# Kernel optimization log

Measured on AMD Instinct MI355X. Metric: run time of the kernel, lower is better.

The kernel has to match this reference:

```python
import jax, jax.numpy as jnp
import numpy as np

NMS_THR = 0.5
SCORE_THR = 0.05
MAX_BOXES = 300
N_ANCHORS = 5000
N_CLASSES = 80
IMG = 640.0  # image size used to scale synthetic box coords


def setup_inputs() -> dict:
    key = jax.random.key(0)
    k1, k2, k3 = jax.random.split(key, 3)
    # build well-formed boxes (x1<=x2, y1<=y2) in a 640x640 image
    c1 = jax.random.uniform(k1, (1, N_ANCHORS, 2), jnp.float32) * IMG
    c2 = jax.random.uniform(k2, (1, N_ANCHORS, 2), jnp.float32) * IMG
    boxes = jnp.concatenate([jnp.minimum(c1, c2), jnp.maximum(c1, c2) + 1.0], axis=-1)
    # classification scores in [0,1], squared to skew toward low values like sigmoid logits
    classification = jax.random.uniform(k3, (1, N_ANCHORS, N_CLASSES), jnp.float32) ** 2
    return {"boxes": boxes, "classification": classification}


def _iou_matrix(b):
    # b: [N,4] as (x1,y1,x2,y2) -> [N,N] pairwise IoU
    x1, y1, x2, y2 = b[:, 0], b[:, 1], b[:, 2], b[:, 3]
    area = (x2 - x1) * (y2 - y1)
    iw = jnp.maximum(jnp.minimum(x2[:, None], x2[None, :]) - jnp.maximum(x1[:, None], x1[None, :]), 0.0)
    ih = jnp.maximum(jnp.minimum(y2[:, None], y2[None, :]) - jnp.maximum(y1[:, None], y1[None, :]), 0.0)
    inter = iw * ih
    union = area[:, None] + area[None, :] - inter
    return inter / jnp.maximum(union, 1e-8)


def _nms_one_class(scores, iou):
    # greedy NMS for one class; scores: [N], iou: [N,N] (shared across classes)
    n = scores.shape[0]
    order = jnp.argsort(-scores)          # descending score order
    valid = scores > SCORE_THR            # per-class score-threshold filter
    idxs = jnp.arange(n)

    def step(carry, oi):
        suppressed, kept, count = carry
        alive = (~suppressed[oi]) & valid[oi] & (count < MAX_BOXES)
        # a kept box suppresses all others with IoU above threshold
        suppressed = suppressed | (alive & (iou[oi] > NMS_THR) & (idxs != oi))
        kept = kept.at[oi].set(alive)
        return (suppressed, kept, count + alive.astype(jnp.int32)), None

    init = (jnp.zeros(n, jnp.bool_), jnp.zeros(n, jnp.bool_), jnp.int32(0))
    (_, kept, _), _ = jax.lax.scan(step, init, order)
    return kept  # [N] bool mask in original index space


def reference(boxes, classification):
    b = boxes[0]             # [N,4]
    cls = classification[0]  # [N,C]
    iou = _iou_matrix(b)     # [N,N], class-independent
    kept = jax.vmap(_nms_one_class, in_axes=(1, None))(cls, iou)  # [C,N]
    # scatter surviving scores back to dense per-class score map (zeros elsewhere)
    selected = jnp.where(kept.T, cls, 0.0)                        # [N,C]
    detections = jnp.concatenate([b, selected], axis=1)           # [N,4+C]
    return detections[None]                                       # [1,N,4+C]
```

## Files before the change

### kernel.cpp

```cpp
#include <hip/hip_runtime.h>

#define N_ANCHORS 5000
#define N_CLASSES 80
#define OUT_COLS  84
#define MAX_BOXES 300
#define SCORE_THR 0.05f

#define LK_PAD    5120
#define NB        4096
#define BLOCK     1024
#define SLOTS     8
#define DONEP     0x40000000u
#define NIW       6
#define NSW       9

typedef unsigned long long u64;
typedef unsigned int u32;

#define WG __HIP_MEMORY_SCOPE_WORKGROUP

__device__ __forceinline__ float readlane_f(float v, int l) {
    return __int_as_float(__builtin_amdgcn_readlane(__float_as_int(v), l));
}
__device__ __forceinline__ u32 aload(u32* p) {
    return __hip_atomic_load(p, __ATOMIC_ACQUIRE, WG);
}
__device__ __forceinline__ u64 aload64(u64* p) {
    return __hip_atomic_load(p, __ATOMIC_ACQUIRE, WG);
}
__device__ __forceinline__ int bucket_of(float s) {
    float u = sqrtf(s);
    int b = (int)((u - 0.2236f) * 5275.0f);
    return (NB - 1) - min(max(b, 0), NB - 1);
}
__device__ __forceinline__ bool iou3(float4 a, float aa, float4 q, float aq) {
    float iw = fmaxf(fminf(a.z, q.z) - fmaxf(a.x, q.x), 0.0f);
    float ih = fmaxf(fminf(a.w, q.w) - fmaxf(a.y, q.y), 0.0f);
    return 3.0f * (iw * ih) > aa + aq;
}

__global__ __launch_bounds__(BLOCK, 1) void nms(const float* __restrict__ cls,
                                                const float4* __restrict__ boxes4,
                                                float* __restrict__ out) {
    __shared__ __align__(16) char SMEM[63680];
    u64*    lk      = (u64*)SMEM;
    u32*    hist    = (u32*)(SMEM + 40960);
    u64*    Iring   = (u64*)(SMEM + 40960);
    float4* Bring   = (float4*)(SMEM + 45056);
    u64*    kout    = (u64*)(SMEM + 53248);
    float4* kbox    = (float4*)(SMEM + 57344);
    float*  karea   = (float*)(SMEM + 62208);
    u64*    KS      = (u64*)(SMEM + 63424);
    u32*    wtot    = (u32*)(SMEM + 63488);
    u64*    flagIK  = (u64*)(SMEM + 63552);
    u32*    flagIK32= (u32*)(SMEM + 63552);
    u64*    progcnt = (u64*)(SMEM + 63616);

    const int c = blockIdx.x;
    const int t = threadIdx.x;
    const int lane = t & 63;
    const int wv = t >> 6;
    const float* boxesf = (const float*)boxes4;

    u32 sb[5];
    #pragma unroll
    for (int m = 0; m < 5; ++m) {
        int j = m * BLOCK + t;
        float v = (j < N_ANCHORS) ? cls[(size_t)j * N_CLASSES + c] : 0.0f;
        sb[m] = (v > SCORE_THR) ? __float_as_uint(v) : 0u;
    }
    for (int i = t; i < N_ANCHORS; i += BLOCK)
        out[(size_t)i * OUT_COLS + 4 + c] = 0.0f;
    if (c < 4)
        for (int i = t; i < N_ANCHORS; i += BLOCK)
            out[(size_t)i * OUT_COLS + c] = boxesf[(size_t)i * 4 + c];

    for (int b = t; b < NB; b += BLOCK) hist[b] = 0u;
    if (t < 304) { kbox[t] = make_float4(1e9f, 1e9f, 1e9f, 1e9f); karea[t] = 1e18f; }
    if (t < SLOTS) flagIK[t] = 0ull;
    if (t == 0) *progcnt = 0ull;
    __syncthreads();
    #pragma unroll
    for (int m = 0; m < 5; ++m)
        if (sb[m]) atomicAdd(&hist[bucket_of(__uint_as_float(sb[m]))], 1u);
    __syncthreads();

    const int hbase = t * 4;
    u32 vals[4]; u32 run = 0;
    #pragma unroll
    for (int k = 0; k < 4; ++k) { run += hist[hbase + k]; vals[k] = run; }
    u32 x = run;
    #pragma unroll
    for (int off = 1; off < 64; off <<= 1) { u32 y = __shfl_up(x, off); if (lane >= off) x += y; }
    if (lane == 63) wtot[wv] = x;
    __syncthreads();
    u32 woff = 0;
    for (int w = 0; w < wv; ++w) woff += wtot[w];
    const u32 exb = woff + x - run;
    #pragma unroll
    for (int k = 0; k < 4; ++k) hist[hbase + k] = exb + (k ? vals[k - 1] : 0u);
    __syncthreads();
    #pragma unroll
    for (int m = 0; m < 5; ++m) {
        if (sb[m]) {
            int j = m * BLOCK + t;
            u32 pos = atomicAdd(&hist[bucket_of(__uint_as_float(sb[m]))], 1u);
            lk[pos] = ((u64)sb[m] << 32) | (u32)(~(u32)j);
        }
    }
    __syncthreads();
    const int total = (int)hist[NB - 1];
    for (int v = total + t; v < LK_PAD; v += BLOCK) lk[v] = 0ull;
    for (int b = hbase; b < hbase + 4; ++b) {
        int s0 = b ? (int)hist[b - 1] : 0;
        int e  = (int)hist[b];
        for (int i = s0 + 1; i < e; ++i) {
            u64 key = lk[i]; int q = i - 1;
            while (q >= s0 && lk[q] < key) { lk[q + 1] = lk[q]; --q; }
            lk[q + 1] = key;
        }
    }
    __syncthreads();
    const int nch = (total + 63) >> 6;

    if (wv >= 1 && wv <= NIW) {
        for (int j = wv - 1; j < nch; j += NIW) {
            const int slot = j & (SLOTS - 1);
            u64 e = lk[j * 64 + lane];
            u32 jj = e ? ~(u32)e : 0u;
            float4 bx = boxes4[jj];
            float ar = (bx.z - bx.x) * (bx.w - bx.y);
            u32 p;
            for (;;) {
                p = (u32)aload64(progcnt);
                if ((int)p >= j - (SLOTS - 1)) break;
                __builtin_amdgcn_s_sleep(2);
            }
            if (p >= DONEP) return;
            u64 word = 0ull;
            #pragma unroll 16
            for (int q = 0; q < 64; ++q) {
                float4 o;
                o.x = readlane_f(bx.x, q); o.y = readlane_f(bx.y, q);
                o.z = readlane_f(bx.z, q); o.w = readlane_f(bx.w, q);
                float aq = readlane_f(ar, q);
                float iw = fmaxf(fminf(bx.z, o.z) - fmaxf(bx.x, o.x), 0.0f);
                float ih = fmaxf(fminf(bx.w, o.w) - fmaxf(bx.y, o.y), 0.0f);
                if (3.0f * (iw * ih) > ar + aq) word |= (1ull << q);
            }
            Iring[slot * 64 + lane] = word;
            if (lane == 0)
                __hip_atomic_store(&flagIK32[slot * 2 + 1], (u32)(j + 1), __ATOMIC_RELEASE, WG);
        }
        return;
    }
    if (wv > NIW) {
        for (int j = wv - (NIW + 1); j < nch; j += NSW) {
            const int slot = j & (SLOTS - 1);
            u64 e = lk[j * 64 + lane];
            bool validL = (e != 0ull);
            u32 jj = validL ? ~(u32)e : 0u;
            float4 bx = boxes4[jj];
            float ar = (bx.z - bx.x) * (bx.w - bx.y);
            u64 pk;
            for (;;) {
                pk = aload64(progcnt);
                if ((int)(u32)pk >= j - (SLOTS - 1)) break;
                __builtin_amdgcn_s_sleep(2);
            }
            if ((u32)pk >= DONEP) return;
            Bring[slot * 64 + lane] = bx;
            bool sup = !validL;
            u32 ka = (u32)(pk >> 32);
            for (u32 r = 0; r < ka; r += 4) {
                float4 q0 = kbox[r], q1 = kbox[r + 1], q2 = kbox[r + 2], q3 = kbox[r + 3];
                float4 a4 = *(const float4*)(karea + r);
                sup = sup | iou3(bx, ar, q0, a4.x) | iou3(bx, ar, q1, a4.y)
                          | iou3(bx, ar, q2, a4.z) | iou3(bx, ar, q3, a4.w);
                if ((r & 28u) == 28u && !__ballot(!sup)) break;
            }
            for (;;) {
                pk = aload64(progcnt);
                if ((int)(u32)pk >= j - 2) break;
                __builtin_amdgcn_s_sleep(1);
            }
            u32 p = (u32)pk;
            u32 kb2 = (u32)(pk >> 32);
            if (kb2 < ka) kb2 = ka;
            u32 r1 = (kb2 + 3) & ~3u;
            for (u32 r = ka & ~3u; r < r1; r += 4) {
                float4 q0 = kbox[r], q1 = kbox[r + 1], q2 = kbox[r + 2], q3 = kbox[r + 3];
                float4 a4 = *(const float4*)(karea + r);
                sup = sup | iou3(bx, ar, q0, a4.x) | iou3(bx, ar, q1, a4.y)
                          | iou3(bx, ar, q2, a4.z) | iou3(bx, ar, q3, a4.w);
            }
            u64 ksf = __ballot(sup);
            if (lane == 0) {
                KS[slot] = ksf;
                __hip_atomic_store(&flagIK32[slot * 2], (u32)(j + 1), __ATOMIC_RELEASE, WG);
            }
            if (p >= DONEP) return;
        }
        return;
    }

    int kept = 0; u32 kcur = 0; bool capped = false;
    u64 kmPrev = 0ull;
    float4 bxPrev = make_float4(0.f, 0.f, 0.f, 0.f);
    float arPrev = 0.f;
    u64 key = lk[lane];
    for (int k = 0; k < nch; ++k) {
        const int slot = k & (SLOTS - 1);
        bool valid = (key != 0ull);
        u32 j = valid ? ~(u32)key : 0u;
        float sc = __uint_as_float((u32)(key >> 32));

        const u64 want = ((u64)(u32)(k + 1) << 32) | (u32)(k + 1);
        while (aload64(&flagIK[slot]) != want) { }
        u64 km = 0ull;
        u64 ks = KS[slot];
        if (ks != ~0ull) {
            float4 bx = Bring[slot * 64 + lane];
            u64 I = Iring[slot * 64 + lane];
            float ar = (bx.z - bx.x) * (bx.w - bx.y);
            bool alive = valid && !((ks >> lane) & 1ull);
            u64 mk = kmPrev;
            while (mk) {
                int pos = __ffsll((long long)mk) - 1; mk &= mk - 1;
                float qx = readlane_f(bxPrev.x, pos), qy = readlane_f(bxPrev.y, pos);
                float qz = readlane_f(bxPrev.z, pos), qw = readlane_f(bxPrev.w, pos);
                float aq = readlane_f(arPrev, pos);
                float iw = fmaxf(fminf(bx.z, qz) - fmaxf(bx.x, qx), 0.0f);
                float ih = fmaxf(fminf(bx.w, qw) - fmaxf(bx.y, qy), 0.0f);
                alive = alive && !(3.0f * (iw * ih) > ar + aq);
            }
            u64 rem = __ballot(alive);
            if (rem) {
                while (rem) {
                    int pos = __ffsll((long long)rem) - 1;
                    km |= 1ull << pos;
                    if (++kept == MAX_BOXES) { capped = true; break; }
                    u32 lo = (u32)__builtin_amdgcn_readlane((int)(u32)I, pos);
                    u32 hi = (u32)__builtin_amdgcn_readlane((int)(u32)(I >> 32), pos);
                    rem &= ~(((u64)hi << 32) | (u64)lo);
                }
                if ((km >> lane) & 1ull) {
                    int rank = (int)__popcll(km & ((1ull << lane) - 1ull));
                    kbox[kcur + rank] = bx;
                    karea[kcur + rank] = ar;
                    kout[kcur + rank] = ((u64)__float_as_uint(sc) << 32) | j;
                }
                kcur += (u32)__popcll(km);
            }
            bxPrev = bx; arPrev = ar;
        }
        kmPrev = km;
        if (capped) break;
        if (lane == 0)
            __hip_atomic_store(progcnt, ((u64)kcur << 32) | (u32)(k + 1),
                               __ATOMIC_RELEASE, WG);
        key = lk[(k + 1) * 64 + lane];
    }
    if (lane == 0)
        __hip_atomic_store(progcnt, ((u64)kcur << 32) | DONEP, __ATOMIC_RELEASE, WG);

    for (u32 i = (u32)lane; i < kcur; i += 64) {
        u64 e = kout[i];
        out[(size_t)((u32)e) * OUT_COLS + 4 + c] = __uint_as_float((u32)(e >> 32));
    }
}

extern "C" void kernel_launch(void* const* d_in, const int* in_sizes, int n_in,
                              void* d_out, int out_size, void* d_ws, size_t ws_size,
                              hipStream_t stream) {
    const float* cls = (const float*)d_in[1];
    float* out = (float*)d_out;
    nms<<<N_CLASSES, BLOCK, 0, stream>>>(cls, (const float4*)d_in[0], out);
}
```

Baseline: 147.1 us.

## Process two 64-box chunks per pipeline step in NMS wavefront pipeline

```diff
diff --git a/kernel.cpp b/kernel.cpp
--- a/kernel.cpp
+++ b/kernel.cpp
@@ -9,21 +9,30 @@
 #define LK_PAD    5120
 #define NB        4096
 #define BLOCK     1024
-#define SLOTS     8
+#define SLOTS     4
 #define DONEP     0x40000000u
 #define NIW       6
 #define NSW       9
 
 typedef unsigned long long u64;
 typedef unsigned int u32;
+typedef unsigned short u16;
 
 #define WG __HIP_MEMORY_SCOPE_WORKGROUP
 
 __device__ __forceinline__ float readlane_f(float v, int l) {
     return __int_as_float(__builtin_amdgcn_readlane(__float_as_int(v), l));
 }
-__device__ __forceinline__ u32 aload(u32* p) {
-    return __hip_atomic_load(p, __ATOMIC_ACQUIRE, WG);
+__device__ __forceinline__ u64 readlane_u64(u64 v, int l) {
+    u32 lo = (u32)__builtin_amdgcn_readlane((int)(u32)v, l);
+    u32 hi = (u32)__builtin_amdgcn_readlane((int)(u32)(v >> 32), l);
+    return ((u64)hi << 32) | lo;
+}
+__device__ __forceinline__ float4 bcast4(float4 b, int q) {
+    float4 o;
+    o.x = readlane_f(b.x, q); o.y = readlane_f(b.y, q);
+    o.z = readlane_f(b.z, q); o.w = readlane_f(b.w, q);
+    return o;
 }
 __device__ __forceinline__ u64 aload64(u64* p) {
     return __hip_atomic_load(p, __ATOMIC_ACQUIRE, WG);
@@ -42,19 +51,19 @@
 __global__ __launch_bounds__(BLOCK, 1) void nms(const float* __restrict__ cls,
                                                 const float4* __restrict__ boxes4,
                                                 float* __restrict__ out) {
-    __shared__ __align__(16) char SMEM[63680];
+    __shared__ __align__(16) char SMEM[63552];
     u64*    lk      = (u64*)SMEM;
     u32*    hist    = (u32*)(SMEM + 40960);
     u64*    Iring   = (u64*)(SMEM + 40960);
     float4* Bring   = (float4*)(SMEM + 45056);
-    u64*    kout    = (u64*)(SMEM + 53248);
+    u16*    kout16  = (u16*)(SMEM + 53248);
+    u64*    KS      = (u64*)(SMEM + 53856);
     float4* kbox    = (float4*)(SMEM + 57344);
     float*  karea   = (float*)(SMEM + 62208);
-    u64*    KS      = (u64*)(SMEM + 63424);
-    u32*    wtot    = (u32*)(SMEM + 63488);
-    u64*    flagIK  = (u64*)(SMEM + 63552);
-    u32*    flagIK32= (u32*)(SMEM + 63552);
-    u64*    progcnt = (u64*)(SMEM + 63616);
+    u32*    wtot    = (u32*)(SMEM + 63424);
+    u64*    flagIK  = (u64*)(SMEM + 63488);
+    u32*    flagIK32= (u32*)(SMEM + 63488);
+    u64*    progcnt = (u64*)(SMEM + 63520);
 
     const int c = blockIdx.x;
     const int t = threadIdx.x;
@@ -121,152 +130,179 @@
         }
     }
     __syncthreads();
-    const int nch = (total + 63) >> 6;
+    const int nsteps = (total + 127) >> 7;
 
     if (wv >= 1 && wv <= NIW) {
-        for (int j = wv - 1; j < nch; j += NIW) {
-            const int slot = j & (SLOTS - 1);
-            u64 e = lk[j * 64 + lane];
-            u32 jj = e ? ~(u32)e : 0u;
-            float4 bx = boxes4[jj];
-            float ar = (bx.z - bx.x) * (bx.w - bx.y);
+        for (int s = wv - 1; s < nsteps; s += NIW) {
+            const int slot = s & (SLOTS - 1);
+            u64 eA = lk[s * 128 + lane], eB = lk[s * 128 + 64 + lane];
+            u32 jA = eA ? ~(u32)eA : 0u, jB = eB ? ~(u32)eB : 0u;
+            float4 bA = boxes4[jA], bB = boxes4[jB];
+            float aA = (bA.z - bA.x) * (bA.w - bA.y);
+            float aB = (bB.z - bB.x) * (bB.w - bB.y);
+            u64 AA = 0ull, BB = 0ull;
+            #pragma unroll 16
+            for (int q = 0; q < 64; ++q) {
+                float4 oA = bcast4(bA, q); float qaA = readlane_f(aA, q);
+                float4 oB = bcast4(bB, q); float qaB = readlane_f(aB, q);
+                if (iou3(bA, aA, oA, qaA)) AA |= 1ull << q;
+                if (iou3(bB, aB, oB, qaB)) BB |= 1ull << q;
+            }
             u32 p;
             for (;;) {
                 p = (u32)aload64(progcnt);
-                if ((int)p >= j - (SLOTS - 1)) break;
+                if ((int)p >= s - (SLOTS - 1)) break;
                 __builtin_amdgcn_s_sleep(2);
             }
             if (p >= DONEP) return;
-            u64 word = 0ull;
-            #pragma unroll 16
-            for (int q = 0; q < 64; ++q) {
-                float4 o;
-                o.x = readlane_f(bx.x, q); o.y = readlane_f(bx.y, q);
-                o.z = readlane_f(bx.z, q); o.w = readlane_f(bx.w, q);
-                float aq = readlane_f(ar, q);
-                float iw = fmaxf(fminf(bx.z, o.z) - fmaxf(bx.x, o.x), 0.0f);
-                float ih = fmaxf(fminf(bx.w, o.w) - fmaxf(bx.y, o.y), 0.0f);
-                if (3.0f * (iw * ih) > ar + aq) word |= (1ull << q);
-            }
-            Iring[slot * 64 + lane] = word;
+            Iring[(slot * 64 + lane) * 2]     = AA;
+            Iring[(slot * 64 + lane) * 2 + 1] = BB;
             if (lane == 0)
-                __hip_atomic_store(&flagIK32[slot * 2 + 1], (u32)(j + 1), __ATOMIC_RELEASE, WG);
+                __hip_atomic_store(&flagIK32[slot * 2 + 1], (u32)(s + 1), __ATOMIC_RELEASE, WG);
         }
         return;
     }
     if (wv > NIW) {
-        for (int j = wv - (NIW + 1); j < nch; j += NSW) {
-            const int slot = j & (SLOTS - 1);
-            u64 e = lk[j * 64 + lane];
-            bool validL = (e != 0ull);
-            u32 jj = validL ? ~(u32)e : 0u;
-            float4 bx = boxes4[jj];
-            float ar = (bx.z - bx.x) * (bx.w - bx.y);
-            u64 pk;
+        for (int s = wv - (NIW + 1); s < nsteps; s += NSW) {
+            const int slot = s & (SLOTS - 1);
+            u64 eA = lk[s * 128 + lane], eB = lk[s * 128 + 64 + lane];
+            bool vA = (eA != 0ull), vB = (eB != 0ull);
+            u32 jA = vA ? ~(u32)eA : 0u, jB = vB ? ~(u32)eB : 0u;
+            float4 bA = boxes4[jA], bB = boxes4[jB];
+            float aA = (bA.z - bA.x) * (bA.w - bA.y);
+            float aB = (bB.z - bB.x) * (bB.w - bB.y);
+            bool supA = !vA, supB = !vB;
+            bool allsup = false;
+            u64 pk = aload64(progcnt);
+            u32 kn = (u32)(pk >> 32), done = 0;
+            {
+                u32 r1 = (kn + 3) & ~3u;
+                for (u32 r = done; r < r1; r += 4) {
+                    float4 q0 = kbox[r], q1 = kbox[r+1], q2 = kbox[r+2], q3 = kbox[r+3];
+                    float4 a4 = *(const float4*)(karea + r);
+                    supA = supA | iou3(bA,aA,q0,a4.x) | iou3(bA,aA,q1,a4.y)
+                                | iou3(bA,aA,q2,a4.z) | iou3(bA,aA,q3,a4.w);
+                    supB = supB | iou3(bB,aB,q0,a4.x) | iou3(bB,aB,q1,a4.y)
+                                | iou3(bB,aB,q2,a4.z) | iou3(bB,aB,q3,a4.w);
+                    if (((r >> 2) & 7u) == 7u && !__ballot(!(supA && supB))) { allsup = true; break; }
+                }
+                done = kn & ~3u;
+            }
             for (;;) {
                 pk = aload64(progcnt);
-                if ((int)(u32)pk >= j - (SLOTS - 1)) break;
+                if ((int)(u32)pk >= s - (SLOTS - 1)) break;
                 __builtin_amdgcn_s_sleep(2);
             }
             if ((u32)pk >= DONEP) return;
-            Bring[slot * 64 + lane] = bx;
-            bool sup = !validL;
-            u32 ka = (u32)(pk >> 32);
-            for (u32 r = 0; r < ka; r += 4) {
-                float4 q0 = kbox[r], q1 = kbox[r + 1], q2 = kbox[r + 2], q3 = kbox[r + 3];
-                float4 a4 = *(const float4*)(karea + r);
-                sup = sup | iou3(bx, ar, q0, a4.x) | iou3(bx, ar, q1, a4.y)
-                          | iou3(bx, ar, q2, a4.z) | iou3(bx, ar, q3, a4.w);
-                if ((r & 28u) == 28u && !__ballot(!sup)) break;
-            }
-            for (;;) {
+            Bring[slot * 128 + lane] = bA;
+            Bring[slot * 128 + 64 + lane] = bB;
+            while (!allsup) {
+                kn = (u32)(pk >> 32);
+                u32 r1 = (kn + 3) & ~3u;
+                for (u32 r = done; r < r1; r += 4) {
+                    float4 q0 = kbox[r], q1 = kbox[r+1], q2 = kbox[r+2], q3 = kbox[r+3];
+                    float4 a4 = *(const float4*)(karea + r);
+                    supA = supA | iou3(bA,aA,q0,a4.x) | iou3(bA,aA,q1,a4.y)
+                                | iou3(bA,aA,q2,a4.z) | iou3(bA,aA,q3,a4.w);
+                    supB = supB | iou3(bB,aB,q0,a4.x) | iou3(bB,aB,q1,a4.y)
+                                | iou3(bB,aB,q2,a4.z) | iou3(bB,aB,q3,a4.w);
+                    if (((r >> 2) & 7u) == 7u && !__ballot(!(supA && supB))) { allsup = true; break; }
+                }
+                if (allsup) break;
+                done = kn & ~3u;
+                if ((int)(u32)pk >= s - 1) break;
                 pk = aload64(progcnt);
-                if ((int)(u32)pk >= j - 2) break;
-                __builtin_amdgcn_s_sleep(1);
-            }
-            u32 p = (u32)pk;
-            u32 kb2 = (u32)(pk >> 32);
-            if (kb2 < ka) kb2 = ka;
-            u32 r1 = (kb2 + 3) & ~3u;
-            for (u32 r = ka & ~3u; r < r1; r += 4) {
-                float4 q0 = kbox[r], q1 = kbox[r + 1], q2 = kbox[r + 2], q3 = kbox[r + 3];
-                float4 a4 = *(const float4*)(karea + r);
-                sup = sup | iou3(bx, ar, q0, a4.x) | iou3(bx, ar, q1, a4.y)
-                          | iou3(bx, ar, q2, a4.z) | iou3(bx, ar, q3, a4.w);
-            }
-            u64 ksf = __ballot(sup);
+            }
+            u64 KSA = __ballot(supA), KSB = __ballot(supB);
             if (lane == 0) {
-                KS[slot] = ksf;
-                __hip_atomic_store(&flagIK32[slot * 2], (u32)(j + 1), __ATOMIC_RELEASE, WG);
-            }
-            if (p >= DONEP) return;
+                KS[slot * 2] = KSA; KS[slot * 2 + 1] = KSB;
+                __hip_atomic_store(&flagIK32[slot * 2], (u32)(s + 1), __ATOMIC_RELEASE, WG);
+            }
+            if ((u32)pk >= DONEP) return;
         }
         return;
     }
 
     int kept = 0; u32 kcur = 0; bool capped = false;
-    u64 kmPrev = 0ull;
-    float4 bxPrev = make_float4(0.f, 0.f, 0.f, 0.f);
-    float arPrev = 0.f;
-    u64 key = lk[lane];
-    for (int k = 0; k < nch; ++k) {
-        const int slot = k & (SLOTS - 1);
-        bool valid = (key != 0ull);
-        u32 j = valid ? ~(u32)key : 0u;
-        float sc = __uint_as_float((u32)(key >> 32));
-
-        const u64 want = ((u64)(u32)(k + 1) << 32) | (u32)(k + 1);
+    u64 kmPrevA = 0ull, kmPrevB = 0ull;
+    float4 bxPvA = make_float4(0,0,0,0), bxPvB = make_float4(0,0,0,0);
+    float arPvA = 0.f, arPvB = 0.f;
+    u64 keyA = lk[lane], keyB = lk[64 + lane];
+    for (int s = 0; s < nsteps; ++s) {
+        const int slot = s & (SLOTS - 1);
+        bool vA = (keyA != 0ull), vB = (keyB != 0ull);
+
+        const u64 want = ((u64)(u32)(s + 1) << 32) | (u32)(s + 1);
         while (aload64(&flagIK[slot]) != want) { }
-        u64 km = 0ull;
-        u64 ks = KS[slot];
-        if (ks != ~0ull) {
-            float4 bx = Bring[slot * 64 + lane];
-            u64 I = Iring[slot * 64 + lane];
-            float ar = (bx.z - bx.x) * (bx.w - bx.y);
-            bool alive = valid && !((ks >> lane) & 1ull);
-            u64 mk = kmPrev;
+        u64 ksA = KS[slot * 2], ksB = KS[slot * 2 + 1];
+        u64 kmA = 0ull, kmB = 0ull;
+        if ((ksA & ksB) != ~0ull) {
+            float4 bxA = Bring[slot * 128 + lane];
+            float4 bxB = Bring[slot * 128 + 64 + lane];
+            u64 IAA = Iring[(slot * 64 + lane) * 2];
+            u64 IBB = Iring[(slot * 64 + lane) * 2 + 1];
+            float arA = (bxA.z - bxA.x) * (bxA.w - bxA.y);
+            float arB = (bxB.z - bxB.x) * (bxB.w - bxB.y);
+            bool alA = vA && !((ksA >> lane) & 1ull);
+            bool alB = vB && !((ksB >> lane) & 1ull);
+            u64 mk = kmPrevA;
             while (mk) {
-                int pos = __ffsll((long long)mk) - 1; mk &= mk - 1;
-                float qx = readlane_f(bxPrev.x, pos), qy = readlane_f(bxPrev.y, pos);
-                float qz = readlane_f(bxPrev.z, pos), qw = readlane_f(bxPrev.w, pos);
-                float aq = readlane_f(arPrev, pos);
-                float iw = fmaxf(fminf(bx.z, qz) - fmaxf(bx.x, qx), 0.0f);
-                float ih = fmaxf(fminf(bx.w, qw) - fmaxf(bx.y, qy), 0.0f);
-                alive = alive && !(3.0f * (iw * ih) > ar + aq);
-            }
-            u64 rem = __ballot(alive);
-            if (rem) {
-                while (rem) {
-                    int pos = __ffsll((long long)rem) - 1;
-                    km |= 1ull << pos;
+                int p = __ffsll((long long)mk) - 1; mk &= mk - 1;
+                float4 q = bcast4(bxPvA, p); float qa = readlane_f(arPvA, p);
+                alA = alA && !iou3(bxA, arA, q, qa);
+                alB = alB && !iou3(bxB, arB, q, qa);
+            }
+            mk = kmPrevB;
+            while (mk) {
+                int p = __ffsll((long long)mk) - 1; mk &= mk - 1;
+                float4 q = bcast4(bxPvB, p); float qa = readlane_f(arPvB, p);
+                alA = alA && !iou3(bxA, arA, q, qa);
+                alB = alB && !iou3(bxB, arB, q, qa);
+            }
+            u64 remA = __ballot(alA), remB = __ballot(alB);
+            while (remA | remB) {
+                if (remA) {
+                    int p = __ffsll((long long)remA) - 1;
+                    kmA |= 1ull << p;
                     if (++kept == MAX_BOXES) { capped = true; break; }
-                    u32 lo = (u32)__builtin_amdgcn_readlane((int)(u32)I, pos);
-                    u32 hi = (u32)__builtin_amdgcn_readlane((int)(u32)(I >> 32), pos);
-                    rem &= ~(((u64)hi << 32) | (u64)lo);
+                    remA &= ~readlane_u64(IAA, p);
+                    float4 q = bcast4(bxA, p); float qa = readlane_f(arA, p);
+                    remB &= ~__ballot(iou3(bxB, arB, q, qa));
+                } else {
+                    int p = __ffsll((long long)remB) - 1;
+                    kmB |= 1ull << p;
+                    if (++kept == MAX_BOXES) { capped = true; break; }
+                    remB &= ~readlane_u64(IBB, p);
                 }
-                if ((km >> lane) & 1ull) {
-                    int rank = (int)__popcll(km & ((1ull << lane) - 1ull));
-                    kbox[kcur + rank] = bx;
-                    karea[kcur + rank] = ar;
-                    kout[kcur + rank] = ((u64)__float_as_uint(sc) << 32) | j;
-                }
-                kcur += (u32)__popcll(km);
-            }
-            bxPrev = bx; arPrev = ar;
-        }
-        kmPrev = km;
+            }
+            u32 cA = (u32)__popcll(kmA);
+            if ((kmA >> lane) & 1ull) {
+                int rk = (int)__popcll(kmA & ((1ull << lane) - 1ull));
+                kbox[kcur + rk] = bxA; karea[kcur + rk] = arA;
+                kout16[kcur + rk] = (u16)(s * 128 + lane);
+            }
+            if ((kmB >> lane) & 1ull) {
+                int rk = (int)cA + (int)__popcll(kmB & ((1ull << lane) - 1ull));
+                kbox[kcur + rk] = bxB; karea[kcur + rk] = arB;
+                kout16[kcur + rk] = (u16)(s * 128 + 64 + lane);
+            }
+            kcur += cA + (u32)__popcll(kmB);
+            bxPvA = bxA; arPvA = arA; bxPvB = bxB; arPvB = arB;
+        }
+        kmPrevA = kmA; kmPrevB = kmB;
         if (capped) break;
         if (lane == 0)
-            __hip_atomic_store(progcnt, ((u64)kcur << 32) | (u32)(k + 1),
+            __hip_atomic_store(progcnt, ((u64)kcur << 32) | (u32)(s + 1),
                                __ATOMIC_RELEASE, WG);
-        key = lk[(k + 1) * 64 + lane];
+        int nb = (s + 1 < nsteps) ? (s + 1) * 128 : 0;
+        keyA = lk[nb + lane]; keyB = lk[nb + 64 + lane];
     }
     if (lane == 0)
         __hip_atomic_store(progcnt, ((u64)kcur << 32) | DONEP, __ATOMIC_RELEASE, WG);
 
     for (u32 i = (u32)lane; i < kcur; i += 64) {
-        u64 e = kout[i];
-        out[(size_t)((u32)e) * OUT_COLS + 4 + c] = __uint_as_float((u32)(e >> 32));
+        u64 key = lk[kout16[i]];
+        out[(size_t)(~(u32)key) * OUT_COLS + 4 + c] = __uint_as_float((u32)(key >> 32));
     }
 }
 
```

Result: slower. 196.0 us (+33.3%).

## Split NMS into sort kernel and smaller-block scan kernel with u16 sorted indices

Applied to the files above, without the earlier changes.

```diff
diff --git a/kernel.cpp b/kernel.cpp
--- a/kernel.cpp
+++ b/kernel.cpp
@@ -6,24 +6,22 @@
 #define MAX_BOXES 300
 #define SCORE_THR 0.05f
 
-#define LK_PAD    5120
+#define SORT_PAD  5056
+#define SIDX_PAD  5120
 #define NB        4096
-#define BLOCK     1024
 #define SLOTS     8
-#define DONEP     0x40000000u
-#define NIW       6
-#define NSW       9
+#define DONEP     0x40000000
+#define NIW       3
+#define NSW       4
 
 typedef unsigned long long u64;
 typedef unsigned int u32;
+typedef unsigned short u16;
 
 #define WG __HIP_MEMORY_SCOPE_WORKGROUP
 
 __device__ __forceinline__ float readlane_f(float v, int l) {
     return __int_as_float(__builtin_amdgcn_readlane(__float_as_int(v), l));
-}
-__device__ __forceinline__ u32 aload(u32* p) {
-    return __hip_atomic_load(p, __ATOMIC_ACQUIRE, WG);
 }
 __device__ __forceinline__ u64 aload64(u64* p) {
     return __hip_atomic_load(p, __ATOMIC_ACQUIRE, WG);
@@ -35,50 +33,39 @@
 }
 __device__ __forceinline__ bool iou3(float4 a, float aa, float4 q, float aq) {
     float iw = fmaxf(fminf(a.z, q.z) - fmaxf(a.x, q.x), 0.0f);
-    float ih = fmaxf(fminf(a.w, q.w) - fmaxf(a.y, q.y), 0.0f);
+    float ih = fminf(a.w, q.w) - fmaxf(a.y, q.y);
     return 3.0f * (iw * ih) > aa + aq;
 }
 
-__global__ __launch_bounds__(BLOCK, 1) void nms(const float* __restrict__ cls,
-                                                const float4* __restrict__ boxes4,
-                                                float* __restrict__ out) {
-    __shared__ __align__(16) char SMEM[63680];
-    u64*    lk      = (u64*)SMEM;
-    u32*    hist    = (u32*)(SMEM + 40960);
-    u64*    Iring   = (u64*)(SMEM + 40960);
-    float4* Bring   = (float4*)(SMEM + 45056);
-    u64*    kout    = (u64*)(SMEM + 53248);
-    float4* kbox    = (float4*)(SMEM + 57344);
-    float*  karea   = (float*)(SMEM + 62208);
-    u64*    KS      = (u64*)(SMEM + 63424);
-    u32*    wtot    = (u32*)(SMEM + 63488);
-    u64*    flagIK  = (u64*)(SMEM + 63552);
-    u32*    flagIK32= (u32*)(SMEM + 63552);
-    u64*    progcnt = (u64*)(SMEM + 63616);
+__global__ __launch_bounds__(1024) void nms_sort(const float* __restrict__ cls,
+                                                 const float* __restrict__ boxesf,
+                                                 float* __restrict__ out,
+                                                 u16* __restrict__ sidx,
+                                                 u32* __restrict__ totals) {
+    __shared__ __align__(16) char SMEM[56896];
+    u64* lk   = (u64*)SMEM;
+    u32* hist = (u32*)(SMEM + 40448);
+    u32* wtot = (u32*)(SMEM + 56832);
 
     const int c = blockIdx.x;
     const int t = threadIdx.x;
     const int lane = t & 63;
     const int wv = t >> 6;
-    const float* boxesf = (const float*)boxes4;
 
     u32 sb[5];
     #pragma unroll
     for (int m = 0; m < 5; ++m) {
-        int j = m * BLOCK + t;
+        int j = m * 1024 + t;
         float v = (j < N_ANCHORS) ? cls[(size_t)j * N_CLASSES + c] : 0.0f;
         sb[m] = (v > SCORE_THR) ? __float_as_uint(v) : 0u;
     }
-    for (int i = t; i < N_ANCHORS; i += BLOCK)
+    for (int i = t; i < N_ANCHORS; i += 1024)
         out[(size_t)i * OUT_COLS + 4 + c] = 0.0f;
     if (c < 4)
-        for (int i = t; i < N_ANCHORS; i += BLOCK)
+        for (int i = t; i < N_ANCHORS; i += 1024)
             out[(size_t)i * OUT_COLS + c] = boxesf[(size_t)i * 4 + c];
 
-    for (int b = t; b < NB; b += BLOCK) hist[b] = 0u;
-    if (t < 304) { kbox[t] = make_float4(1e9f, 1e9f, 1e9f, 1e9f); karea[t] = 1e18f; }
-    if (t < SLOTS) flagIK[t] = 0ull;
-    if (t == 0) *progcnt = 0ull;
+    for (int b = t; b < NB; b += 1024) hist[b] = 0u;
     __syncthreads();
     #pragma unroll
     for (int m = 0; m < 5; ++m)
@@ -103,14 +90,14 @@
     #pragma unroll
     for (int m = 0; m < 5; ++m) {
         if (sb[m]) {
-            int j = m * BLOCK + t;
+            int j = m * 1024 + t;
             u32 pos = atomicAdd(&hist[bucket_of(__uint_as_float(sb[m]))], 1u);
             lk[pos] = ((u64)sb[m] << 32) | (u32)(~(u32)j);
         }
     }
     __syncthreads();
     const int total = (int)hist[NB - 1];
-    for (int v = total + t; v < LK_PAD; v += BLOCK) lk[v] = 0ull;
+    for (int v = total + t; v < SORT_PAD; v += 1024) lk[v] = 0ull;
     for (int b = hbase; b < hbase + 4; ++b) {
         int s0 = b ? (int)hist[b - 1] : 0;
         int e  = (int)hist[b];
@@ -121,22 +108,51 @@
         }
     }
     __syncthreads();
+    u16* sc_ = sidx + (size_t)c * SIDX_PAD;
+    for (int v = t; v < SIDX_PAD; v += 1024) {
+        u64 e = (v < SORT_PAD) ? lk[v] : 0ull;
+        sc_[v] = e ? (u16)(~(u32)e) : (u16)0xFFFF;
+    }
+    if (t == 0) totals[c] = (u32)total;
+}
+
+__global__ __launch_bounds__(512, 1) void nms_scan(const float* __restrict__ cls,
+                                                   const float4* __restrict__ boxes4,
+                                                   const u16* __restrict__ sidx,
+                                                   const u32* __restrict__ totals,
+                                                   float* __restrict__ out) {
+    __shared__ __align__(16) char SMEM[19200];
+    u64*    Iring   = (u64*)SMEM;
+    float4* Bring   = (float4*)(SMEM + 4096);
+    float4* kbox    = (float4*)(SMEM + 12288);
+    float*  karea   = (float*)(SMEM + 17152);
+    u16*    kout16  = (u16*)(SMEM + 18368);
+    u64*    KS      = (u64*)(SMEM + 18976);
+    u32*    KBa     = (u32*)(SMEM + 19040);
+    u64*    flagIK  = (u64*)(SMEM + 19072);
+    u32*    flagIK32= (u32*)(SMEM + 19072);
+    u64*    progcnt = (u64*)(SMEM + 19136);
+
+    const int c = blockIdx.x;
+    const int t = threadIdx.x;
+    const int lane = t & 63;
+    const int wv = t >> 6;
+    const u16* sc_ = sidx + (size_t)c * SIDX_PAD;
+
+    if (t < 304) { kbox[t] = make_float4(1e9f, 1e9f, 1e9f, 1e9f); karea[t] = 1e18f; }
+    if (t < SLOTS) flagIK[t] = 0ull;
+    if (t == 0) *progcnt = 0ull;
+    __syncthreads();
+    const int total = (int)totals[c];
     const int nch = (total + 63) >> 6;
 
     if (wv >= 1 && wv <= NIW) {
         for (int j = wv - 1; j < nch; j += NIW) {
             const int slot = j & (SLOTS - 1);
-            u64 e = lk[j * 64 + lane];
-            u32 jj = e ? ~(u32)e : 0u;
+            u16 g = sc_[j * 64 + lane];
+            u32 jj = (g != 0xFFFF) ? g : 0u;
             float4 bx = boxes4[jj];
             float ar = (bx.z - bx.x) * (bx.w - bx.y);
-            u32 p;
-            for (;;) {
-                p = (u32)aload64(progcnt);
-                if ((int)p >= j - (SLOTS - 1)) break;
-                __builtin_amdgcn_s_sleep(2);
-            }
-            if (p >= DONEP) return;
             u64 word = 0ull;
             #pragma unroll 16
             for (int q = 0; q < 64; ++q) {
@@ -145,9 +161,16 @@
                 o.z = readlane_f(bx.z, q); o.w = readlane_f(bx.w, q);
                 float aq = readlane_f(ar, q);
                 float iw = fmaxf(fminf(bx.z, o.z) - fmaxf(bx.x, o.x), 0.0f);
-                float ih = fmaxf(fminf(bx.w, o.w) - fmaxf(bx.y, o.y), 0.0f);
+                float ih = fminf(bx.w, o.w) - fmaxf(bx.y, o.y);
                 if (3.0f * (iw * ih) > ar + aq) word |= (1ull << q);
             }
+            u32 p;
+            for (;;) {
+                p = (u32)aload64(progcnt);
+                if ((int)p >= j - (SLOTS - 1)) break;
+                __builtin_amdgcn_s_sleep(2);
+            }
+            if (p >= DONEP) return;
             Iring[slot * 64 + lane] = word;
             if (lane == 0)
                 __hip_atomic_store(&flagIK32[slot * 2 + 1], (u32)(j + 1), __ATOMIC_RELEASE, WG);
@@ -157,9 +180,9 @@
     if (wv > NIW) {
         for (int j = wv - (NIW + 1); j < nch; j += NSW) {
             const int slot = j & (SLOTS - 1);
-            u64 e = lk[j * 64 + lane];
-            bool validL = (e != 0ull);
-            u32 jj = validL ? ~(u32)e : 0u;
+            u16 g = sc_[j * 64 + lane];
+            bool validL = (g != 0xFFFF);
+            u32 jj = validL ? g : 0u;
             float4 bx = boxes4[jj];
             float ar = (bx.z - bx.x) * (bx.w - bx.y);
             u64 pk;
@@ -171,71 +194,63 @@
             if ((u32)pk >= DONEP) return;
             Bring[slot * 64 + lane] = bx;
             bool sup = !validL;
-            u32 ka = (u32)(pk >> 32);
-            for (u32 r = 0; r < ka; r += 4) {
+            u32 done = 0; bool alldead = false;
+            for (;;) {
+                u32 kn = (u32)(pk >> 32);
+                u32 r4 = kn & ~3u;
+                for (u32 r = done; r < r4; r += 4) {
+                    float4 q0 = kbox[r], q1 = kbox[r+1], q2 = kbox[r+2], q3 = kbox[r+3];
+                    float4 a4 = *(const float4*)(karea + r);
+                    sup = sup | iou3(bx,ar,q0,a4.x) | iou3(bx,ar,q1,a4.y)
+                              | iou3(bx,ar,q2,a4.z) | iou3(bx,ar,q3,a4.w);
+                    if (((r >> 2) & 7u) == 7u && !__ballot(!sup)) { alldead = true; break; }
+                }
+                if (alldead) break;
+                for (u32 r = r4; r < kn; ++r)
+                    sup = sup | iou3(bx, ar, kbox[r], karea[r]);
+                done = r4;
+                if ((int)(u32)pk >= j - 2) break;
+                __builtin_amdgcn_s_sleep(1);
+                pk = aload64(progcnt);
+            }
+            u64 ksf = __ballot(sup);
+            if (lane == 0) {
+                KS[slot] = ksf; KBa[slot] = (u32)(pk >> 32);
+                __hip_atomic_store(&flagIK32[slot * 2], (u32)(j + 1), __ATOMIC_RELEASE, WG);
+            }
+            if ((u32)pk >= DONEP) return;
+        }
+        return;
+    }
+
+    __builtin_amdgcn_s_setprio(3);
+    int kept = 0; u32 kcur = 0; bool capped = false;
+    u16 key = (nch > 0) ? sc_[lane] : (u16)0xFFFF;
+    for (int k = 0; k < nch; ++k) {
+        const int slot = k & (SLOTS - 1);
+        bool valid = (key != 0xFFFF);
+        u32 j = valid ? key : 0u;
+
+        const u64 want = ((u64)(u32)(k + 1) << 32) | (u32)(k + 1);
+        while (aload64(&flagIK[slot]) != want) { }
+        u64 ks = KS[slot];
+        u32 kb = KBa[slot];
+        float4 bx = Bring[slot * 64 + lane];
+        u64 I = Iring[slot * 64 + lane];
+        if (ks != ~0ull) {
+            float ar = (bx.z - bx.x) * (bx.w - bx.y);
+            bool alive = valid && !((ks >> lane) & 1ull);
+            u32 r1 = (kcur + 3) & ~3u;
+            for (u32 r = kb & ~3u; r < r1; r += 4) {
                 float4 q0 = kbox[r], q1 = kbox[r + 1], q2 = kbox[r + 2], q3 = kbox[r + 3];
                 float4 a4 = *(const float4*)(karea + r);
-                sup = sup | iou3(bx, ar, q0, a4.x) | iou3(bx, ar, q1, a4.y)
-                          | iou3(bx, ar, q2, a4.z) | iou3(bx, ar, q3, a4.w);
-                if ((r & 28u) == 28u && !__ballot(!sup)) break;
-            }
-            for (;;) {
-                pk = aload64(progcnt);
-                if ((int)(u32)pk >= j - 2) break;
-                __builtin_amdgcn_s_sleep(1);
-            }
-            u32 p = (u32)pk;
-            u32 kb2 = (u32)(pk >> 32);
-            if (kb2 < ka) kb2 = ka;
-            u32 r1 = (kb2 + 3) & ~3u;
-            for (u32 r = ka & ~3u; r < r1; r += 4) {
-                float4 q0 = kbox[r], q1 = kbox[r + 1], q2 = kbox[r + 2], q3 = kbox[r + 3];
-                float4 a4 = *(const float4*)(karea + r);
-                sup = sup | iou3(bx, ar, q0, a4.x) | iou3(bx, ar, q1, a4.y)
-                          | iou3(bx, ar, q2, a4.z) | iou3(bx, ar, q3, a4.w);
-            }
-            u64 ksf = __ballot(sup);
-            if (lane == 0) {
-                KS[slot] = ksf;
-                __hip_atomic_store(&flagIK32[slot * 2], (u32)(j + 1), __ATOMIC_RELEASE, WG);
-            }
-            if (p >= DONEP) return;
-        }
-        return;
-    }
-
-    int kept = 0; u32 kcur = 0; bool capped = false;
-    u64 kmPrev = 0ull;
-    float4 bxPrev = make_float4(0.f, 0.f, 0.f, 0.f);
-    float arPrev = 0.f;
-    u64 key = lk[lane];
-    for (int k = 0; k < nch; ++k) {
-        const int slot = k & (SLOTS - 1);
-        bool valid = (key != 0ull);
-        u32 j = valid ? ~(u32)key : 0u;
-        float sc = __uint_as_float((u32)(key >> 32));
-
-        const u64 want = ((u64)(u32)(k + 1) << 32) | (u32)(k + 1);
-        while (aload64(&flagIK[slot]) != want) { }
-        u64 km = 0ull;
-        u64 ks = KS[slot];
-        if (ks != ~0ull) {
-            float4 bx = Bring[slot * 64 + lane];
-            u64 I = Iring[slot * 64 + lane];
-            float ar = (bx.z - bx.x) * (bx.w - bx.y);
-            bool alive = valid && !((ks >> lane) & 1ull);
-            u64 mk = kmPrev;
-            while (mk) {
-                int pos = __ffsll((long long)mk) - 1; mk &= mk - 1;
-                float qx = readlane_f(bxPrev.x, pos), qy = readlane_f(bxPrev.y, pos);
-                float qz = readlane_f(bxPrev.z, pos), qw = readlane_f(bxPrev.w, pos);
-                float aq = readlane_f(arPrev, pos);
-                float iw = fmaxf(fminf(bx.z, qz) - fmaxf(bx.x, qx), 0.0f);
-                float ih = fmaxf(fminf(bx.w, qw) - fmaxf(bx.y, qy), 0.0f);
-                alive = alive && !(3.0f * (iw * ih) > ar + aq);
+                bool s = iou3(bx, ar, q0, a4.x) | iou3(bx, ar, q1, a4.y)
+                       | iou3(bx, ar, q2, a4.z) | iou3(bx, ar, q3, a4.w);
+                alive = alive && !s;
             }
             u64 rem = __ballot(alive);
             if (rem) {
+                u64 km = 0ull;
                 while (rem) {
                     int pos = __ffsll((long long)rem) - 1;
                     km |= 1ull << pos;
@@ -248,32 +263,35 @@
                     int rank = (int)__popcll(km & ((1ull << lane) - 1ull));
                     kbox[kcur + rank] = bx;
                     karea[kcur + rank] = ar;
-                    kout[kcur + rank] = ((u64)__float_as_uint(sc) << 32) | j;
+                    kout16[kcur + rank] = (u16)j;
                 }
                 kcur += (u32)__popcll(km);
             }
-            bxPrev = bx; arPrev = ar;
-        }
-        kmPrev = km;
+        }
         if (capped) break;
         if (lane == 0)
             __hip_atomic_store(progcnt, ((u64)kcur << 32) | (u32)(k + 1),
                                __ATOMIC_RELEASE, WG);
-        key = lk[(k + 1) * 64 + lane];
+        if (k + 1 < nch) key = sc_[(k + 1) * 64 + lane];
     }
     if (lane == 0)
         __hip_atomic_store(progcnt, ((u64)kcur << 32) | DONEP, __ATOMIC_RELEASE, WG);
+    __builtin_amdgcn_s_setprio(0);
 
     for (u32 i = (u32)lane; i < kcur; i += 64) {
-        u64 e = kout[i];
-        out[(size_t)((u32)e) * OUT_COLS + 4 + c] = __uint_as_float((u32)(e >> 32));
+        u32 idx = kout16[i];
+        out[(size_t)idx * OUT_COLS + 4 + c] = cls[(size_t)idx * N_CLASSES + c];
     }
 }
 
 extern "C" void kernel_launch(void* const* d_in, const int* in_sizes, int n_in,
                               void* d_out, int out_size, void* d_ws, size_t ws_size,
                               hipStream_t stream) {
-    const float* cls = (const float*)d_in[1];
+    const float* boxes = (const float*)d_in[0];
+    const float* cls   = (const float*)d_in[1];
     float* out = (float*)d_out;
-    nms<<<N_CLASSES, BLOCK, 0, stream>>>(cls, (const float4*)d_in[0], out);
-}
+    u16* sidx   = (u16*)d_ws;
+    u32* totals = (u32*)((char*)d_ws + N_CLASSES * SIDX_PAD * 2);
+    nms_sort<<<N_CLASSES, 1024, 0, stream>>>(cls, boxes, out, sidx, totals);
+    nms_scan<<<N_CLASSES, 512, 0, stream>>>(cls, (const float4*)boxes, sidx, totals, out);
+}
```

Result: no change. 149.0 us (+1.3%).
